# Optimization experiments

Measured on AMD Instinct MI355X. Metric: run time of the kernel, lower is better.

## Reference

```python
import jax, jax.numpy as jnp
import numpy as np

N = 50000       # nodes
E = 800000      # edges (before self-loops)
NFEAT = 256
NHID = 16       # per-head hidden dim
HEADS = 8
NCLASS = 16
NEG_SLOPE = 0.2  # PyG GATConv default leaky-relu slope


def setup_inputs() -> dict:
    key = jax.random.key(0)
    ks = jax.random.split(key, 10)
    s = 0.05  # weight scale for numerical sanity
    return {
        "x": jax.random.normal(ks[0], (N, NFEAT), jnp.float32),
        "edge_index": jax.random.randint(ks[1], (2, E), 0, N, dtype=jnp.int32),
        "W1": jax.random.normal(ks[2], (NFEAT, HEADS * NHID), jnp.float32) * s,
        "att_src1": jax.random.normal(ks[3], (HEADS, NHID), jnp.float32) * s,
        "att_dst1": jax.random.normal(ks[4], (HEADS, NHID), jnp.float32) * s,
        "b1": jnp.zeros((HEADS * NHID,), jnp.float32),
        "W2": jax.random.normal(ks[5], (HEADS * NHID, NCLASS), jnp.float32) * s,
        "att_src2": jax.random.normal(ks[6], (1, NCLASS), jnp.float32) * s,
        "att_dst2": jax.random.normal(ks[7], (1, NCLASS), jnp.float32) * s,
        "b2": jnp.zeros((NCLASS,), jnp.float32),
    }


def gat_conv(x, edge_index, W, a_src, a_dst, b, heads, out_c, concat):
    """Faithful PyG GATConv (eval mode: dropout off, add_self_loops=True)."""
    n = x.shape[0]
    loop = jnp.arange(n, dtype=edge_index.dtype)
    src = jnp.concatenate([edge_index[0], loop])  # [E+N]
    dst = jnp.concatenate([edge_index[1], loop])  # [E+N]
    h = (x @ W).reshape(n, heads, out_c)          # [N, H, C]
    # per-node attention logits
    alpha_src = jnp.einsum('nhc,hc->nh', h, a_src)  # [N, H]
    alpha_dst = jnp.einsum('nhc,hc->nh', h, a_dst)  # [N, H]
    e = jax.nn.leaky_relu(alpha_src[src] + alpha_dst[dst], NEG_SLOPE)  # [E+N, H]
    # segment softmax over incoming edges of each dst node (self-loop guarantees nonempty)
    m = jax.lax.stop_gradient(jax.ops.segment_max(e, dst, num_segments=n))
    p = jnp.exp(e - m[dst])
    denom = jax.ops.segment_sum(p, dst, num_segments=n)
    a = p / denom[dst]                              # [E+N, H]
    out = jax.ops.segment_sum(a[:, :, None] * h[src], dst, num_segments=n)  # [N, H, C]
    out = out.reshape(n, heads * out_c) if concat else out.mean(axis=1)
    return out + b


def reference(x, edge_index, W1, att_src1, att_dst1, b1, W2, att_src2, att_dst2, b2):
    h1 = jax.nn.elu(gat_conv(x, edge_index, W1, att_src1, att_dst1, b1, HEADS, NHID, True))
    return gat_conv(h1, edge_index, W2, att_src2, att_dst2, b2, 1, NCLASS, False)
```

## Files before the change

kernel.cpp:

```cpp
#include <hip/hip_runtime.h>
#include <hip/hip_bf16.h>

#define NNODES 50000
#define NEDGES 800000
#define NFEATS 256
#define NHID 16
#define HEADS 8
#define NCLS 16
#define NEG_SLOPE 0.2f
#define TOTE (NEDGES + NNODES)
#define RSTRIDE 64
#define NBUCK 196
#define NPB 256
#define BCAP 4864
#define S1_EPT 16
#define BIN_BLOCKS ((TOTE + 4095) / 4096)
#define GSTRIDE 16
#define GEMM1_BLOCKS ((NNODES + 127) / 128)

typedef __attribute__((ext_vector_type(8))) short short8;
typedef __attribute__((ext_vector_type(4))) float floatx4;

static __device__ __forceinline__ short f2bf(float f) {
    __hip_bfloat16 b = __float2bfloat16(f);
    return *reinterpret_cast<short*>(&b);
}

#define AS1 __attribute__((address_space(1)))
#define AS3 __attribute__((address_space(3)))

static __device__ __forceinline__ void ld_lds16(const void* g, void* l) {
#if __has_builtin(__builtin_amdgcn_global_load_lds)
    __builtin_amdgcn_global_load_lds((const AS1 void*)g, (AS3 void*)l, 16, 0, 0);
#endif
}


__global__ __launch_bounds__(256) void k_bin(const int* __restrict__ ei,
                                             int* __restrict__ gcnt, int* __restrict__ barr,
                                             const float* __restrict__ W,
                                             const float* __restrict__ a_s,
                                             const float* __restrict__ a_d,
                                             short* __restrict__ Wsw) {
    int tid = threadIdx.x;
    if (blockIdx.x >= BIN_BLOCKS) {
        int t = (blockIdx.x - BIN_BLOCKS) * 256 + tid;
        if (t >= 4608) return;
        short8 b;
        if (t < 4096) {
            int kc = t >> 9, nt = (t >> 6) & 7, lane = t & 63;
            int quad = lane >> 4, lo = lane & 15;
#pragma unroll
            for (int j = 0; j < 8; j++)
                b[j] = f2bf(W[(size_t)(kc * 32 + quad * 8 + j) * 128 + nt * 16 + lo]);
        } else {
            int t2 = t - 4096;
            int kc = t2 >> 6, lane = t2 & 63;
            int quad = lane >> 4, lo = lane & 15;
            int h = lo & 7;
            const float* av = (lo < 8) ? (a_s + h * 16) : (a_d + h * 16);
#pragma unroll
            for (int j = 0; j < 8; j++) {
                int k = kc * 32 + quad * 8 + j;
                float acc = 0.f;
#pragma unroll
                for (int c = 0; c < 16; c++) acc += W[(size_t)k * 128 + h * 16 + c] * av[c];
                b[j] = f2bf(acc);
            }
        }
        *(short8*)(Wsw + (size_t)t * 8) = b;
        return;
    }

    __shared__ int lcnt[NBUCK], lbase[NBUCK];
    if (tid < NBUCK) lcnt[tid] = 0;
    __syncthreads();
    int e0 = blockIdx.x * (256 * S1_EPT) + tid;
    int s[S1_EPT], d[S1_EPT], rk[S1_EPT];
#pragma unroll
    for (int k = 0; k < S1_EPT; k++) {
        int e = e0 + k * 256;
        bool v = e < TOTE;
        int ss = 0, dd = 0;
        if (v) {
            if (e < NEDGES) { ss = ei[e]; dd = ei[NEDGES + e]; }
            else            { ss = e - NEDGES; dd = ss; }
        }
        s[k] = ss; d[k] = dd;
        rk[k] = v ? atomicAdd(&lcnt[dd >> 8], 1) : -1;
    }
    __syncthreads();
    if (tid < NBUCK) lbase[tid] = lcnt[tid] ? atomicAdd(&gcnt[tid * GSTRIDE], lcnt[tid]) : 0;
    __syncthreads();
#pragma unroll
    for (int k = 0; k < S1_EPT; k++) {
        if (rk[k] >= 0) {
            int b = d[k] >> 8;
            int pos = lbase[b] + rk[k];
            if (pos < BCAP)
                barr[(size_t)b * BCAP + pos] = ((d[k] & 255) << 16) | s[k];
        }
    }
}


__global__ __launch_bounds__(256) void k_mid(const int* __restrict__ gcnt,
                                             const int* __restrict__ barr,
                                             int* __restrict__ cnt, unsigned short* __restrict__ csr,
                                             const float* __restrict__ x,
                                             const short* __restrict__ Wsw,
                                             __hip_bfloat16* __restrict__ h1,
                                             float* __restrict__ as1, float* __restrict__ ad1) {
    __shared__ short smem[32768];
    int tid = threadIdx.x;

    if (blockIdx.x < NBUCK) {
        int* lcnt = (int*)smem;
        unsigned short* lcsr = (unsigned short*)smem + 512;
        int b = blockIdx.x;
        lcnt[tid] = 0;
        __syncthreads();
        int n = min(gcnt[b * GSTRIDE], BCAP);
        int nodeBase = b << 8;
        for (int i = tid; i < n; i += 256) {
            int e = barr[(size_t)b * BCAP + i];
            int ln = e >> 16;
            int r = atomicAdd(&lcnt[ln], 1);
            if (r < RSTRIDE) lcsr[ln * 65 + r] = (unsigned short)(e & 0xFFFF);
        }
        __syncthreads();
        int node = nodeBase + tid;
        if (node < NNODES) cnt[node] = min(lcnt[tid], RSTRIDE);
        for (int i = tid; i < NPB * RSTRIDE; i += 256) {
            int ln = i >> 6;
            int nn = nodeBase + ln;
            if (nn < NNODES && (i & 63) < min(lcnt[ln], RSTRIDE))
                csr[(size_t)nodeBase * RSTRIDE + i] = lcsr[ln * 65 + (i & 63)];
        }
        return;
    }

    short* bsw = smem;
    int bid  = blockIdx.x - NBUCK;
    int wave = tid >> 6;
    int lane = tid & 63;
    int quad = lane >> 4;
    int lo   = lane & 15;

#if __has_builtin(__builtin_amdgcn_global_load_lds)
    {
        const char* gsrc = (const char*)Wsw + (size_t)wave * 1024 + (size_t)lane * 16;
        char* ldst = (char*)bsw + wave * 1024;
#pragma unroll
        for (int it = 0; it < 16; it++)
            ld_lds16(gsrc + it * 4096, ldst + it * 4096);
    }
#else
    {
        const uint4* g4 = (const uint4*)Wsw;
        uint4* l4 = (uint4*)bsw;
#pragma unroll
        for (int it = 0; it < 16; it++) l4[it * 256 + tid] = g4[it * 256 + tid];
    }
#endif
    short8 wafr[8];
#pragma unroll
    for (int kc = 0; kc < 8; kc++)
        wafr[kc] = *(const short8*)(Wsw + (size_t)(4096 + kc * 64 + lane) * 8);
    __syncthreads();

    int rowBase = bid * 128 + wave * 32;
    const float* xa[2];
#pragma unroll
    for (int mt = 0; mt < 2; mt++) {
        int row = rowBase + mt * 16 + lo;
        row = (row < NNODES) ? row : (NNODES - 1);
        xa[mt] = x + (size_t)row * 256 + quad * 8;
    }

    floatx4 acc[2][8], accA[2];
#pragma unroll
    for (int mt = 0; mt < 2; mt++) {
        accA[mt] = (floatx4){0.f, 0.f, 0.f, 0.f};
#pragma unroll
        for (int nt = 0; nt < 8; nt++) acc[mt][nt] = (floatx4){0.f, 0.f, 0.f, 0.f};
    }

    float4 a0[2], a1[2];
#pragma unroll
    for (int mt = 0; mt < 2; mt++) {
        a0[mt] = *(const float4*)(xa[mt]);
        a1[mt] = *(const float4*)(xa[mt] + 4);
    }

    for (int kc = 0; kc < 8; kc++) {
        float4 n0[2], n1[2];
        if (kc < 7) {
#pragma unroll
            for (int mt = 0; mt < 2; mt++) {
                n0[mt] = *(const float4*)(xa[mt] + (kc + 1) * 32);
                n1[mt] = *(const float4*)(xa[mt] + (kc + 1) * 32 + 4);
            }
        }
        short8 afr[2];
#pragma unroll
        for (int mt = 0; mt < 2; mt++) {
            union { short8 s; __hip_bfloat162 h[4]; } u;
            u.h[0] = __float22bfloat162_rn(make_float2(a0[mt].x, a0[mt].y));
            u.h[1] = __float22bfloat162_rn(make_float2(a0[mt].z, a0[mt].w));
            u.h[2] = __float22bfloat162_rn(make_float2(a1[mt].x, a1[mt].y));
            u.h[3] = __float22bfloat162_rn(make_float2(a1[mt].z, a1[mt].w));
            afr[mt] = u.s;
        }
#pragma unroll
        for (int nt = 0; nt < 8; nt++) {
            short8 bfr = *(const short8*)&bsw[((kc * 8 + nt) * 64 + lane) * 8];
            acc[0][nt] = __builtin_amdgcn_mfma_f32_16x16x32_bf16(afr[0], bfr, acc[0][nt], 0, 0, 0);
            acc[1][nt] = __builtin_amdgcn_mfma_f32_16x16x32_bf16(afr[1], bfr, acc[1][nt], 0, 0, 0);
        }
        accA[0] = __builtin_amdgcn_mfma_f32_16x16x32_bf16(afr[0], wafr[kc], accA[0], 0, 0, 0);
        accA[1] = __builtin_amdgcn_mfma_f32_16x16x32_bf16(afr[1], wafr[kc], accA[1], 0, 0, 0);
#pragma unroll
        for (int mt = 0; mt < 2; mt++) { a0[mt] = n0[mt]; a1[mt] = n1[mt]; }
    }

#pragma unroll
    for (int mt = 0; mt < 2; mt++)
#pragma unroll
        for (int nt = 0; nt < 8; nt++)
#pragma unroll
            for (int reg = 0; reg < 4; reg++) {
                int row = rowBase + mt * 16 + quad * 4 + reg;
                int col = nt * 16 + lo;
                if (row < NNODES)
                    h1[(size_t)row * 128 + col] = __float2bfloat16(acc[mt][nt][reg]);
            }
#pragma unroll
    for (int mt = 0; mt < 2; mt++)
#pragma unroll
        for (int reg = 0; reg < 4; reg++) {
            int row = rowBase + mt * 16 + quad * 4 + reg;
            if (row < NNODES) {
                float v = accA[mt][reg];
                if (lo < 8) as1[(size_t)row * 8 + lo] = v;
                else        ad1[(size_t)row * 8 + (lo - 8)] = v;
            }
        }
}


__global__ __launch_bounds__(256) void k_aggA(const int* __restrict__ cnt,
                                              const unsigned short* __restrict__ csr,
                                              const __hip_bfloat16* __restrict__ h1,
                                              const float* __restrict__ as1, const float* __restrict__ ad1,
                                              const float* __restrict__ b1,
                                              const float* __restrict__ W2,
                                              const float* __restrict__ a_s2,
                                              const float* __restrict__ a_d2,
                                              float* __restrict__ h2,
                                              float* __restrict__ as2, float* __restrict__ ad2) {
    __shared__ float w2s[2176];
    int tid  = threadIdx.x;
#pragma unroll
    for (int i = 0; i < 8; i++) {
        int e = i * 256 + tid;
        w2s[(e >> 4) * 17 + (e & 15)] = W2[e];
    }
    __syncthreads();

    int node = blockIdx.x * 4 + (tid >> 6);
    int lane = tid & 63;
    int cl   = lane & 15;
    int slot = lane >> 4;
    int head = cl >> 1;
    int deg  = min(cnt[node], RSTRIDE);
    float adst = ad1[node * 8 + head];
    int rowv = csr[node * RSTRIDE + lane];

    float acc[8] = {0.f, 0.f, 0.f, 0.f, 0.f, 0.f, 0.f, 0.f};
    float s = 0.f;
    for (int i2 = 0; i2 < deg; i2 += 16) {
        float p[4];
        union { short8 v; __hip_bfloat162 h[4]; } u[4];
#pragma unroll
        for (int t = 0; t < 4; t++) {
            int ii = i2 + slot + t * 4;
            int src = __shfl(rowv, ii & 63);
            p[t] = 0.f;
            u[t].v = (short8){0, 0, 0, 0, 0, 0, 0, 0};
            if (ii < deg) {
                u[t].v = *(const short8*)(h1 + (size_t)src * 128 + cl * 8);
                float e = as1[src * 8 + head] + adst;
                e = (e > 0.f) ? e : NEG_SLOPE * e;
                p[t] = __expf(e);
            }
        }
        s += (p[0] + p[1]) + (p[2] + p[3]);
#pragma unroll
        for (int t = 0; t < 4; t++)
#pragma unroll
            for (int q = 0; q < 4; q++) {
                float2 f = __bfloat1622float2(u[t].h[q]);
                acc[q * 2]     = fmaf(p[t], f.x, acc[q * 2]);
                acc[q * 2 + 1] = fmaf(p[t], f.y, acc[q * 2 + 1]);
            }
    }

#pragma unroll
    for (int q = 0; q < 8; q++) {
        acc[q] += __shfl_xor(acc[q], 16);
        acc[q] += __shfl_xor(acc[q], 32);
    }
    s += __shfl_xor(s, 16);
    s += __shfl_xor(s, 32);

    float is = 1.f / s;
    float4 b1a = *(const float4*)(b1 + cl * 8);
    float4 b1b = *(const float4*)(b1 + cl * 8 + 4);
    float v[8];
    v[0] = acc[0] * is + b1a.x; v[1] = acc[1] * is + b1a.y;
    v[2] = acc[2] * is + b1a.z; v[3] = acc[3] * is + b1a.w;
    v[4] = acc[4] * is + b1b.x; v[5] = acc[5] * is + b1b.y;
    v[6] = acc[6] * is + b1b.z; v[7] = acc[7] * is + b1b.w;
#pragma unroll
    for (int q = 0; q < 8; q++) v[q] = (v[q] > 0.f) ? v[q] : (__expf(v[q]) - 1.f);

    float outp = 0.f;
#pragma unroll
    for (int j = 0; j < 32; j++) {
        float vk = __shfl(v[j & 7], slot * 4 + (j >> 3));
        float wk = w2s[(slot * 32 + j) * 17 + cl];
        outp = fmaf(vk, wk, outp);
    }
    outp += __shfl_xor(outp, 16);
    outp += __shfl_xor(outp, 32);
    if (slot == 0) h2[(size_t)node * 16 + cl] = outp;

    float sv = outp * a_s2[cl];
    float dv = outp * a_d2[cl];
#pragma unroll
    for (int o = 1; o <= 8; o <<= 1) {
        sv += __shfl_xor(sv, o);
        dv += __shfl_xor(dv, o);
    }
    if (lane == 0) { as2[node] = sv; ad2[node] = dv; }
}


__global__ __launch_bounds__(256) void k_agg2(const int* __restrict__ cnt,
                                              const unsigned short* __restrict__ csr,
                                              const float* __restrict__ h2, const float* __restrict__ as2,
                                              const float* __restrict__ ad2, const float* __restrict__ b2,
                                              float* __restrict__ out) {
    int node = blockIdx.x * 4 + (threadIdx.x >> 6);
    int lane = threadIdx.x & 63;
    int c4   = lane & 3;
    int slot = lane >> 2;
    int deg  = min(cnt[node], RSTRIDE);
    float adst = ad2[node];
    int rowv = csr[node * RSTRIDE + lane];

    float4 acc = make_float4(0.f, 0.f, 0.f, 0.f);
    float s = 0.f;
    for (int i2 = 0; i2 < deg; i2 += 32) {
        int ia = i2 + slot;
        int ib = ia + 16;
        int sa = __shfl(rowv, ia & 63);
        int sb = __shfl(rowv, ib & 63);
        float p0 = 0.f, p1 = 0.f;
        float4 r0 = make_float4(0.f, 0.f, 0.f, 0.f);
        float4 r1 = make_float4(0.f, 0.f, 0.f, 0.f);
        if (ia < deg) {
            r0 = *(const float4*)(h2 + (size_t)sa * 16 + c4 * 4);
            float e = as2[sa] + adst;
            e = (e > 0.f) ? e : NEG_SLOPE * e;
            p0 = __expf(e);
        }
        if (ib < deg) {
            r1 = *(const float4*)(h2 + (size_t)sb * 16 + c4 * 4);
            float e = as2[sb] + adst;
            e = (e > 0.f) ? e : NEG_SLOPE * e;
            p1 = __expf(e);
        }
        s += p0 + p1;
        acc.x = fmaf(p0, r0.x, fmaf(p1, r1.x, acc.x));
        acc.y = fmaf(p0, r0.y, fmaf(p1, r1.y, acc.y));
        acc.z = fmaf(p0, r0.z, fmaf(p1, r1.z, acc.z));
        acc.w = fmaf(p0, r0.w, fmaf(p1, r1.w, acc.w));
    }
#pragma unroll
    for (int o = 4; o <= 32; o <<= 1) {
        acc.x += __shfl_xor(acc.x, o);
        acc.y += __shfl_xor(acc.y, o);
        acc.z += __shfl_xor(acc.z, o);
        acc.w += __shfl_xor(acc.w, o);
        s += __shfl_xor(s, o);
    }
    if (slot == 0) {
        float is = 1.f / s;
        float4 o4;
        o4.x = acc.x * is + b2[c4 * 4 + 0];
        o4.y = acc.y * is + b2[c4 * 4 + 1];
        o4.z = acc.z * is + b2[c4 * 4 + 2];
        o4.w = acc.w * is + b2[c4 * 4 + 3];
        *(float4*)(out + (size_t)node * 16 + c4 * 4) = o4;
    }
}


extern "C" void kernel_launch(void* const* d_in, const int* in_sizes, int n_in,
                              void* d_out, int out_size, void* d_ws, size_t ws_size,
                              hipStream_t stream) {
    const float* x    = (const float*)d_in[0];
    const int*   ei   = (const int*)d_in[1];
    const float* W1   = (const float*)d_in[2];
    const float* a_s1 = (const float*)d_in[3];
    const float* a_d1 = (const float*)d_in[4];
    const float* b1   = (const float*)d_in[5];
    const float* W2   = (const float*)d_in[6];
    const float* a_s2 = (const float*)d_in[7];
    const float* a_d2 = (const float*)d_in[8];
    const float* b2   = (const float*)d_in[9];
    float* out = (float*)d_out;

    char* p = (char*)d_ws;
    auto alloc = [&](size_t bytes) -> char* {
        char* q = p;
        p += (bytes + 255) & ~(size_t)255;
        return q;
    };
    int*  gcnt = (int*)alloc((size_t)NBUCK * GSTRIDE * 4);
    int*  barr = (int*)alloc((size_t)NBUCK * BCAP * 4);
    int*  cnt  = (int*)alloc((size_t)NNODES * 4);
    unsigned short* csr = (unsigned short*)alloc((size_t)NNODES * RSTRIDE * 2);
    short* Wsw = (short*)alloc((size_t)36864 * 2);
    __hip_bfloat16* h1 = (__hip_bfloat16*)alloc((size_t)NNODES * 128 * 2);
    float* as1 = (float*)alloc((size_t)NNODES * 8 * 4);
    float* ad1 = (float*)alloc((size_t)NNODES * 8 * 4);
    float* h2  = (float*)alloc((size_t)NNODES * 16 * 4);
    float* as2 = (float*)barr;
    float* ad2 = (float*)barr + NNODES;

    hipMemsetAsync(gcnt, 0, (size_t)NBUCK * GSTRIDE * 4, stream);
    hipLaunchKernelGGL(k_bin,   dim3(BIN_BLOCKS + 18), dim3(256), 0, stream,
                       ei, gcnt, barr, W1, a_s1, a_d1, Wsw);
    hipLaunchKernelGGL(k_mid,   dim3(NBUCK + GEMM1_BLOCKS), dim3(256), 0, stream,
                       gcnt, barr, cnt, csr, x, Wsw, h1, as1, ad1);
    hipLaunchKernelGGL(k_aggA,  dim3(NNODES / 4), dim3(256), 0, stream,
                       cnt, csr, h1, as1, ad1, b1, W2, a_s2, a_d2, h2, as2, ad2);
    hipLaunchKernelGGL(k_agg2,  dim3(NNODES / 4), dim3(256), 0, stream, cnt, csr, h2, as2, ad2, b2, out);
}
```

Baseline: 208.6 us.

## Map four nodes per wavefront in layer-1 aggregation and use LDS matvec

The layer-1 aggregation kernel now gives each wavefront four nodes, one per 16-lane group, instead of one node split across four edge slots. This removes the cross-slot shuffle reductions and cuts the grid to a quarter of its former size. Each group loops to the maximum degree among its four nodes, so lanes with shorter neighbor lists sit idle. The W2 projection now writes the ELU activations to LDS and does a float4 dot product against a transposed W2 tile, replacing the per-element shuffles.

```diff
diff --git a/kernel.cpp b/kernel.cpp
--- a/kernel.cpp
+++ b/kernel.cpp
@@ -259,82 +259,90 @@
                                               const float* __restrict__ a_d2,
                                               float* __restrict__ h2,
                                               float* __restrict__ as2, float* __restrict__ ad2) {
-    __shared__ float w2s[2176];
-    int tid  = threadIdx.x;
+    __shared__ float w2t[16 * 132];
+    __shared__ float vbuf[4 * 4 * 132];
+    int tid = threadIdx.x;
 #pragma unroll
     for (int i = 0; i < 8; i++) {
         int e = i * 256 + tid;
-        w2s[(e >> 4) * 17 + (e & 15)] = W2[e];
+        w2t[(e & 15) * 132 + (e >> 4)] = W2[e];
     }
     __syncthreads();
 
-    int node = blockIdx.x * 4 + (tid >> 6);
-    int lane = tid & 63;
-    int cl   = lane & 15;
-    int slot = lane >> 4;
-    int head = cl >> 1;
-    int deg  = min(cnt[node], RSTRIDE);
+    int wavid = tid >> 6;
+    int lane  = tid & 63;
+    int cl    = lane & 15;
+    int nd    = lane >> 4;
+    int node  = (blockIdx.x * 4 + wavid) * 4 + nd;
+    int head  = cl >> 1;
+    int deg   = min(cnt[node], RSTRIDE);
     float adst = ad1[node * 8 + head];
-    int rowv = csr[node * RSTRIDE + lane];
+    int rs = node * RSTRIDE;
+    int rowv[4];
+#pragma unroll
+    for (int r = 0; r < 4; r++) rowv[r] = csr[rs + cl + 16 * r];
+    int md = deg;
+    md = max(md, __shfl_xor(md, 16));
+    md = max(md, __shfl_xor(md, 32));
 
     float acc[8] = {0.f, 0.f, 0.f, 0.f, 0.f, 0.f, 0.f, 0.f};
     float s = 0.f;
-    for (int i2 = 0; i2 < deg; i2 += 16) {
-        float p[4];
-        union { short8 v; __hip_bfloat162 h[4]; } u[4];
-#pragma unroll
-        for (int t = 0; t < 4; t++) {
-            int ii = i2 + slot + t * 4;
-            int src = __shfl(rowv, ii & 63);
-            p[t] = 0.f;
-            u[t].v = (short8){0, 0, 0, 0, 0, 0, 0, 0};
-            if (ii < deg) {
-                u[t].v = *(const short8*)(h1 + (size_t)src * 128 + cl * 8);
-                float e = as1[src * 8 + head] + adst;
-                e = (e > 0.f) ? e : NEG_SLOPE * e;
-                p[t] = __expf(e);
+#pragma unroll
+    for (int r = 0; r < 4; r++) {
+        int rbase = r << 4;
+        if (rbase >= md) break;
+        int lim = min(16, md - rbase);
+        for (int i2 = 0; i2 < lim; i2 += 4) {
+            float p[4];
+            union { short8 v; __hip_bfloat162 h[4]; } u[4];
+#pragma unroll
+            for (int t = 0; t < 4; t++) {
+                int idx = rbase + i2 + t;
+                int src = __shfl(rowv[r], (lane & 48) | ((i2 + t) & 15));
+                p[t] = 0.f;
+                u[t].v = (short8){0, 0, 0, 0, 0, 0, 0, 0};
+                if (idx < deg) {
+                    u[t].v = *(const short8*)(h1 + (size_t)src * 128 + cl * 8);
+                    float e = as1[src * 8 + head] + adst;
+                    e = (e > 0.f) ? e : NEG_SLOPE * e;
+                    p[t] = __expf(e);
+                }
             }
-        }
-        s += (p[0] + p[1]) + (p[2] + p[3]);
-#pragma unroll
-        for (int t = 0; t < 4; t++)
-#pragma unroll
-            for (int q = 0; q < 4; q++) {
-                float2 f = __bfloat1622float2(u[t].h[q]);
-                acc[q * 2]     = fmaf(p[t], f.x, acc[q * 2]);
-                acc[q * 2 + 1] = fmaf(p[t], f.y, acc[q * 2 + 1]);
-            }
-    }
-
+            s += (p[0] + p[1]) + (p[2] + p[3]);
+#pragma unroll
+            for (int t = 0; t < 4; t++)
+#pragma unroll
+                for (int q = 0; q < 4; q++) {
+                    float2 f = __bfloat1622float2(u[t].h[q]);
+                    acc[q * 2]     = fmaf(p[t], f.x, acc[q * 2]);
+                    acc[q * 2 + 1] = fmaf(p[t], f.y, acc[q * 2 + 1]);
+                }
+        }
+    }
+    float is = 1.f / s;
+    float v[8];
 #pragma unroll
     for (int q = 0; q < 8; q++) {
-        acc[q] += __shfl_xor(acc[q], 16);
-        acc[q] += __shfl_xor(acc[q], 32);
-    }
-    s += __shfl_xor(s, 16);
-    s += __shfl_xor(s, 32);
-
-    float is = 1.f / s;
-    float4 b1a = *(const float4*)(b1 + cl * 8);
-    float4 b1b = *(const float4*)(b1 + cl * 8 + 4);
-    float v[8];
-    v[0] = acc[0] * is + b1a.x; v[1] = acc[1] * is + b1a.y;
-    v[2] = acc[2] * is + b1a.z; v[3] = acc[3] * is + b1a.w;
-    v[4] = acc[4] * is + b1b.x; v[5] = acc[5] * is + b1b.y;
-    v[6] = acc[6] * is + b1b.z; v[7] = acc[7] * is + b1b.w;
-#pragma unroll
-    for (int q = 0; q < 8; q++) v[q] = (v[q] > 0.f) ? v[q] : (__expf(v[q]) - 1.f);
-
+        float t = acc[q] * is + b1[cl * 8 + q];
+        v[q] = (t > 0.f) ? t : (__expf(t) - 1.f);
+    }
+    float* vb = &vbuf[(wavid * 4 + nd) * 132 + cl * 8];
+    *(float4*)vb       = make_float4(v[0], v[1], v[2], v[3]);
+    *(float4*)(vb + 4) = make_float4(v[4], v[5], v[6], v[7]);
+
+    const float* vrow = &vbuf[(wavid * 4 + nd) * 132];
+    const float* wrow = &w2t[cl * 132];
     float outp = 0.f;
 #pragma unroll
-    for (int j = 0; j < 32; j++) {
-        float vk = __shfl(v[j & 7], slot * 4 + (j >> 3));
-        float wk = w2s[(slot * 32 + j) * 17 + cl];
-        outp = fmaf(vk, wk, outp);
-    }
-    outp += __shfl_xor(outp, 16);
-    outp += __shfl_xor(outp, 32);
-    if (slot == 0) h2[(size_t)node * 16 + cl] = outp;
+    for (int j = 0; j < 128; j += 4) {
+        float4 vv = *(const float4*)(vrow + j);
+        float4 ww = *(const float4*)(wrow + j);
+        outp = fmaf(vv.x, ww.x, outp);
+        outp = fmaf(vv.y, ww.y, outp);
+        outp = fmaf(vv.z, ww.z, outp);
+        outp = fmaf(vv.w, ww.w, outp);
+    }
+    h2[(size_t)node * 16 + cl] = outp;
 
     float sv = outp * a_s2[cl];
     float dv = outp * a_d2[cl];
@@ -343,7 +351,7 @@
         sv += __shfl_xor(sv, o);
         dv += __shfl_xor(dv, o);
     }
-    if (lane == 0) { as2[node] = sv; ad2[node] = dv; }
+    if (cl == 0) { as2[node] = sv; ad2[node] = dv; }
 }
 
 
@@ -442,11 +450,11 @@
     float* ad2 = (float*)barr + NNODES;
 
     hipMemsetAsync(gcnt, 0, (size_t)NBUCK * GSTRIDE * 4, stream);
-    hipLaunchKernelGGL(k_bin,   dim3(BIN_BLOCKS + 18), dim3(256), 0, stream,
+    hipLaunchKernelGGL(k_bin,  dim3(BIN_BLOCKS + 18), dim3(256), 0, stream,
                        ei, gcnt, barr, W1, a_s1, a_d1, Wsw);
-    hipLaunchKernelGGL(k_mid,   dim3(NBUCK + GEMM1_BLOCKS), dim3(256), 0, stream,
+    hipLaunchKernelGGL(k_mid,  dim3(NBUCK + GEMM1_BLOCKS), dim3(256), 0, stream,
                        gcnt, barr, cnt, csr, x, Wsw, h1, as1, ad1);
-    hipLaunchKernelGGL(k_aggA,  dim3(NNODES / 4), dim3(256), 0, stream,
+    hipLaunchKernelGGL(k_aggA, dim3(NNODES / 16), dim3(256), 0, stream,
                        cnt, csr, h1, as1, ad1, b1, W2, a_s2, a_d2, h2, as2, ad2);
-    hipLaunchKernelGGL(k_agg2,  dim3(NNODES / 4), dim3(256), 0, stream, cnt, csr, h2, as2, ad2, b2, out);
-}
+    hipLaunchKernelGGL(k_agg2, dim3(NNODES / 4), dim3(256), 0, stream, cnt, csr, h2, as2, ad2, b2, out);
+}
```

After: 191.5 us. -8.2%, faster.
